# Optimization experiments

Measured on AMD Instinct MI355X. Metric: run time of the kernel, lower is better.

The kernel has to match this reference:

```python
import jax, jax.numpy as jnp
import numpy as np

N = 100000     # nodes
E = 1600000    # directed edges
IN, HID, OUT = 128, 64, 64


def setup_inputs() -> dict:
    key = jax.random.key(0)
    k = jax.random.split(key, 6)
    features = jax.random.normal(k[0], (N, IN), dtype=jnp.float32)
    edge_index = jax.random.randint(k[1], (2, E), 0, N, dtype=jnp.int64)
    # Glorot-ish init for linear weights, zeros for bias (PyG GCNConv default)
    W1 = jax.random.normal(k[2], (IN, HID), dtype=jnp.float32) / np.sqrt(IN)
    b1 = jnp.zeros((HID,), dtype=jnp.float32)
    W2 = jax.random.normal(k[3], (HID, OUT), dtype=jnp.float32) / np.sqrt(HID)
    b2 = jnp.zeros((OUT,), dtype=jnp.float32)
    return {"features": features, "edge_index": edge_index, "batch_size": N,
            "W1": W1, "b1": b1, "W2": W2, "b2": b2}


def _gcn_conv(x, W, b, src, dst, n):
    """PyG GCNConv: add self-loops, symmetric deg^-1/2 normalization,
    linear transform then scatter-add aggregation, plus bias."""
    loops = jnp.arange(n, dtype=src.dtype)
    s = jnp.concatenate([src, loops])   # [E+N]
    d = jnp.concatenate([dst, loops])   # [E+N]
    deg = jax.ops.segment_sum(jnp.ones(s.shape, dtype=x.dtype), d, num_segments=n)
    dinv = jnp.where(deg > 0, jax.lax.rsqrt(deg), jnp.zeros_like(deg))
    norm = dinv[s] * dinv[d]            # [E+N]
    h = x @ W                           # [n, out] transform before aggregation
    msg = h[s] * norm[:, None]          # gather + scale  [E+N, out]
    out = jax.ops.segment_sum(msg, d, num_segments=n)  # scatter-add
    return out + b


def reference(features, edge_index, batch_size, W1, b1, W2, b2):
    src, dst = edge_index[0], edge_index[1]
    n = features.shape[0]
    x = _gcn_conv(features, W1, b1, src, dst, n)
    x = jax.nn.relu(x)
    # F.dropout(training=self.training): module is in eval mode -> identity
    x = _gcn_conv(x, W2, b2, src, dst, n)
    return jax.nn.log_softmax(x, axis=1)
```

## Files before the change

kernel.cpp:

```cpp
#include <hip/hip_runtime.h>
#include <hip/hip_fp16.h>
#include <math.h>

#define K1 128
#define C  64
#define SCAN_B 1024

__global__ void detect_kernel(const int* __restrict__ e, int twoE, int* __restrict__ flag) {
    __shared__ int nz;
    if (threadIdx.x == 0) nz = 0;
    __syncthreads();
    int nchk = twoE / 2; if (nchk > 4096) nchk = 4096;
    int bad = 0;
    for (int i = threadIdx.x; i < nchk; i += blockDim.x)
        if (e[2 * i + 1] != 0) bad = 1;
    if (bad) atomicOr(&nz, 1);
    __syncthreads();
    if (threadIdx.x == 0) *flag = nz ? 0 : 1;
}

__device__ __forceinline__ int load_dst(const void* EI, int E, int e, int is64) {
    return is64 ? (int)((const long long*)EI)[(size_t)E + e] : ((const int*)EI)[(size_t)E + e];
}
__device__ __forceinline__ int load_src(const void* EI, int E, int e, int is64) {
    return is64 ? (int)((const long long*)EI)[e] : ((const int*)EI)[e];
}

__global__ __launch_bounds__(256) void hist_kernel(const void* __restrict__ EI, int E,
        const int* __restrict__ flag, int* __restrict__ cnt) {
    const int is64 = *flag;
    for (int e = blockIdx.x * 256 + threadIdx.x; e < E; e += gridDim.x * 256)
        atomicAdd(&cnt[load_dst(EI, E, e, is64)], 1);
}

__global__ __launch_bounds__(SCAN_B) void scan1_kernel(const int* __restrict__ cnt, int n,
        int* __restrict__ ex, int* __restrict__ bsum, float* __restrict__ dinv) {
    __shared__ int s[SCAN_B];
    int i = blockIdx.x * SCAN_B + threadIdx.x;
    int v = (i < n) ? cnt[i] : 0;
    s[threadIdx.x] = v;
    __syncthreads();
    for (int off = 1; off < SCAN_B; off <<= 1) {
        int t = (threadIdx.x >= off) ? s[threadIdx.x - off] : 0;
        __syncthreads();
        s[threadIdx.x] += t;
        __syncthreads();
    }
    if (i < n) {
        ex[i] = s[threadIdx.x] - v;
        dinv[i] = rsqrtf((float)(v + 1));
    }
    if (threadIdx.x == SCAN_B - 1) bsum[blockIdx.x] = s[SCAN_B - 1];
}

__global__ void scan2_kernel(int* __restrict__ bsum, int nb) {
    const int lane = threadIdx.x & 63;
    int acc = 0;
    for (int base = 0; base < nb; base += 64) {
        int v = (base + lane < nb) ? bsum[base + lane] : 0;
        int sc = v;
        #pragma unroll
        for (int off = 1; off < 64; off <<= 1) {
            int t = __shfl_up(sc, off, 64);
            if (lane >= off) sc += t;
        }
        if (base + lane < nb) bsum[base + lane] = acc + sc - v;
        acc += __shfl(sc, 63, 64);
    }
}

__global__ void scan3_kernel(int* __restrict__ ex, const int* __restrict__ bsum,
                             int* __restrict__ fill, int n, int Etot) {
    for (int i = blockIdx.x * blockDim.x + threadIdx.x; i < n; i += gridDim.x * blockDim.x) {
        int v = ex[i] + bsum[i / SCAN_B];
        ex[i] = v;
        fill[i] = v;
    }
    if (blockIdx.x == 0 && threadIdx.x == 0) ex[n] = Etot;
}

__global__ __launch_bounds__(256) void scatter_kernel(const void* __restrict__ EI, int E,
        const int* __restrict__ flag, int* __restrict__ fill, int* __restrict__ csr) {
    const int is64 = *flag;
    for (int e = blockIdx.x * 256 + threadIdx.x; e < E; e += gridDim.x * 256) {
        int d = load_dst(EI, E, e, is64);
        int s = load_src(EI, E, e, is64);
        int pos = atomicAdd(&fill[d], 1);
        csr[pos] = s;
    }
}

template<int K, int R>
__global__ __launch_bounds__(256) void gemm_kernel(const float* __restrict__ X,
        const float* __restrict__ W, const float* __restrict__ dinv,
        __half* __restrict__ G, int n)
{
    __shared__ float Ws[K * C];
    for (int i = threadIdx.x; i < K * C; i += 256) Ws[i] = W[i];
    __syncthreads();
    const int lane = threadIdx.x & 63;
    const int wave = __builtin_amdgcn_readfirstlane((int)(threadIdx.x >> 6));
    const int waves = gridDim.x * 4;
    for (int base = (blockIdx.x * 4 + wave) * R; base < n; base += waves * R) {
        float acc[R];
        #pragma unroll
        for (int r = 0; r < R; ++r) acc[r] = 0.0f;
        if (base + R <= n) {
            for (int k = 0; k < K; ++k) {
                float w = Ws[k * C + lane];
                #pragma unroll
                for (int r = 0; r < R; ++r)
                    acc[r] = fmaf(X[(size_t)(base + r) * K + k], w, acc[r]);
            }
            #pragma unroll
            for (int r = 0; r < R; ++r)
                G[(size_t)(base + r) * C + lane] = __float2half_rn(acc[r] * dinv[base + r]);
        } else {
            for (int r = 0; r < R; ++r) {
                if (base + r >= n) break;
                float a = 0.0f;
                for (int k = 0; k < K; ++k)
                    a = fmaf(X[(size_t)(base + r) * K + k], Ws[k * C + lane], a);
                G[(size_t)(base + r) * C + lane] = __float2half_rn(a * dinv[base + r]);
            }
        }
    }
}

__global__ __launch_bounds__(256) void gather_fused_kernel(const int* __restrict__ rowptr,
        const int* __restrict__ csr, const __half* __restrict__ G,
        const float* __restrict__ dinv, const float* __restrict__ b1,
        const float* __restrict__ W2, __half* __restrict__ G2, int n)
{
    __shared__ __align__(16) float Hrow[4][C];
    const int lane = threadIdx.x & 63;
    const int wv = __builtin_amdgcn_readfirstlane((int)(threadIdx.x >> 6));
    float w[C];
    #pragma unroll
    for (int k = 0; k < C; ++k) w[k] = W2[k * C + lane];
    const float bias = b1[lane];
    const int nwaves = gridDim.x * 4;
    for (int v = __builtin_amdgcn_readfirstlane(blockIdx.x * 4 + wv); v < n; v += nwaves) {
        const int start = __builtin_amdgcn_readfirstlane(rowptr[v]);
        const int end   = __builtin_amdgcn_readfirstlane(rowptr[v + 1]);
        float a0 = __half2float(G[(size_t)v * C + lane]);
        float a1 = 0.f, a2 = 0.f, a3 = 0.f;
        for (int base = start; base < end; base += 64) {
            int m = end - base; if (m > 64) m = 64;
            int idx = (lane < m) ? csr[base + lane] : 0;
            int j = 0;
            for (; j + 4 <= m; j += 4) {
                int s0 = __shfl(idx, j,     64);
                int s1 = __shfl(idx, j + 1, 64);
                int s2 = __shfl(idx, j + 2, 64);
                int s3 = __shfl(idx, j + 3, 64);
                a0 += __half2float(G[(size_t)s0 * C + lane]);
                a1 += __half2float(G[(size_t)s1 * C + lane]);
                a2 += __half2float(G[(size_t)s2 * C + lane]);
                a3 += __half2float(G[(size_t)s3 * C + lane]);
            }
            for (; j < m; ++j) {
                int s = __shfl(idx, j, 64);
                a0 += __half2float(G[(size_t)s * C + lane]);
            }
        }
        float y = fmaf((a0 + a1) + (a2 + a3), dinv[v], bias);
        y = y > 0.f ? y : 0.f;
        Hrow[wv][lane] = y;
        float o = 0.f;
        #pragma unroll
        for (int k0 = 0; k0 < C / 4; ++k0) {
            float4 h4 = *(const float4*)&Hrow[wv][k0 * 4];
            o = fmaf(h4.x, w[4 * k0 + 0], o);
            o = fmaf(h4.y, w[4 * k0 + 1], o);
            o = fmaf(h4.z, w[4 * k0 + 2], o);
            o = fmaf(h4.w, w[4 * k0 + 3], o);
        }
        G2[(size_t)v * C + lane] = __float2half_rn(o * dinv[v]);
    }
}

__global__ __launch_bounds__(256) void gather_ls_kernel(const int* __restrict__ rowptr,
        const int* __restrict__ csr, const __half* __restrict__ G,
        const float* __restrict__ dinv, const float* __restrict__ bias,
        float* __restrict__ Out, int n)
{
    const int lane = threadIdx.x & 63;
    const int v = __builtin_amdgcn_readfirstlane((int)(blockIdx.x * 4 + (threadIdx.x >> 6)));
    if (v >= n) return;
    const int start = __builtin_amdgcn_readfirstlane(rowptr[v]);
    const int end   = __builtin_amdgcn_readfirstlane(rowptr[v + 1]);
    float a0 = __half2float(G[(size_t)v * C + lane]);
    float a1 = 0.f, a2 = 0.f, a3 = 0.f;
    for (int base = start; base < end; base += 64) {
        int m = end - base; if (m > 64) m = 64;
        int idx = (lane < m) ? csr[base + lane] : 0;
        int j = 0;
        for (; j + 4 <= m; j += 4) {
            int s0 = __shfl(idx, j,     64);
            int s1 = __shfl(idx, j + 1, 64);
            int s2 = __shfl(idx, j + 2, 64);
            int s3 = __shfl(idx, j + 3, 64);
            a0 += __half2float(G[(size_t)s0 * C + lane]);
            a1 += __half2float(G[(size_t)s1 * C + lane]);
            a2 += __half2float(G[(size_t)s2 * C + lane]);
            a3 += __half2float(G[(size_t)s3 * C + lane]);
        }
        for (; j < m; ++j) {
            int s = __shfl(idx, j, 64);
            a0 += __half2float(G[(size_t)s * C + lane]);
        }
    }
    float y = fmaf((a0 + a1) + (a2 + a3), dinv[v], bias[lane]);
    float mx = y;
    #pragma unroll
    for (int off = 32; off > 0; off >>= 1) mx = fmaxf(mx, __shfl_xor(mx, off, 64));
    float ex = expf(y - mx);
    float l = ex;
    #pragma unroll
    for (int off = 32; off > 0; off >>= 1) l += __shfl_xor(l, off, 64);
    Out[(size_t)v * C + lane] = y - mx - logf(l);
}

static inline size_t align16(size_t x) { return (x + 15) & ~(size_t)15; }

extern "C" void kernel_launch(void* const* d_in, const int* in_sizes, int n_in,
                              void* d_out, int out_size, void* d_ws, size_t ws_size,
                              hipStream_t stream)
{
    const float* X  = (const float*)d_in[0];
    const void*  EI = d_in[1];
    const float* W1 = (const float*)d_in[3];
    const float* b1 = (const float*)d_in[4];
    const float* W2 = (const float*)d_in[5];
    const float* b2 = (const float*)d_in[6];
    float* Out = (float*)d_out;

    const int n    = in_sizes[0] / K1;
    const int E    = in_sizes[1] / 2;
    const int twoE = 2 * E;
    const int nb   = (n + SCAN_B - 1) / SCAN_B;

    char* ws = (char*)d_ws;
    size_t off = 0;
    int*    csr    = (int*)(ws + off);    off = align16(off + (size_t)E * 4);
    int*    rowptr = (int*)(ws + off);    off = align16(off + (size_t)(n + 1) * 4);
    int*    cnt    = (int*)(ws + off);    off = align16(off + (size_t)n * 4);
    int*    bsum   = (int*)(ws + off);    off = align16(off + (size_t)(nb + 1) * 4);
    int*    flag   = (int*)(ws + off);    off = align16(off + 16);
    float*  dinv   = (float*)(ws + off);  off = align16(off + (size_t)n * 4);
    __half* G      = (__half*)(ws + off); off = align16(off + (size_t)n * C * 2);
    __half* G2     = (__half*)(ws + off); off = align16(off + (size_t)n * C * 2);
    int*    fill   = cnt;

    hipLaunchKernelGGL(detect_kernel, dim3(1), dim3(256), 0, stream, (const int*)EI, twoE, flag);
    hipMemsetAsync(cnt, 0, (size_t)n * 4, stream);

    hipLaunchKernelGGL(hist_kernel,  dim3(1024), dim3(256), 0, stream, EI, E, flag, cnt);
    hipLaunchKernelGGL(scan1_kernel, dim3(nb), dim3(SCAN_B), 0, stream, cnt, n, rowptr, bsum, dinv);
    hipLaunchKernelGGL(scan2_kernel, dim3(1), dim3(64), 0, stream, bsum, nb);
    hipLaunchKernelGGL(scan3_kernel, dim3(1024), dim3(256), 0, stream, rowptr, bsum, fill, n, E);
    hipLaunchKernelGGL(scatter_kernel, dim3(2048), dim3(256), 0, stream, EI, E, flag, fill, csr);

    hipLaunchKernelGGL((gemm_kernel<K1, 8>), dim3(2048), dim3(256), 0, stream, X, W1, dinv, G, n);
    hipLaunchKernelGGL(gather_fused_kernel, dim3(2048), dim3(256), 0, stream,
                       rowptr, csr, G, dinv, b1, W2, G2, n);
    const int ngb = (n + 3) / 4;
    hipLaunchKernelGGL(gather_ls_kernel, dim3(ngb), dim3(256), 0, stream,
                       rowptr, csr, G2, dinv, b2, Out, n);
}
```

Before: 524.7 us.

## Partition histogram and CSR scatter by destination range; unroll gathers by eight

The histogram and scatter kernels now split blocks into eight groups. Each group scans every edge but only performs atomics for destinations in its own node range, which is meant to keep the atomic targets cache-local and reduce contention, at the cost of reading the edge list eight times. The gather loops in both aggregation kernels are shared through a macro and unrolled to eight independent loads and accumulators, to raise memory-level parallelism.

New measurement: 484.2 us. 1.08x faster.

```diff
diff --git a/kernel.cpp b/kernel.cpp
--- a/kernel.cpp
+++ b/kernel.cpp
@@ -5,6 +5,7 @@
 #define K1 128
 #define C  64
 #define SCAN_B 1024
+#define NPART 8
 
 __global__ void detect_kernel(const int* __restrict__ e, int twoE, int* __restrict__ flag) {
     __shared__ int nz;
@@ -27,10 +28,17 @@
 }
 
 __global__ __launch_bounds__(256) void hist_kernel(const void* __restrict__ EI, int E,
-        const int* __restrict__ flag, int* __restrict__ cnt) {
+        const int* __restrict__ flag, int* __restrict__ cnt, int n) {
     const int is64 = *flag;
-    for (int e = blockIdx.x * 256 + threadIdx.x; e < E; e += gridDim.x * 256)
-        atomicAdd(&cnt[load_dst(EI, E, e, is64)], 1);
+    const int part = blockIdx.x & (NPART - 1);
+    const int span = (n + NPART - 1) / NPART;
+    const int lo = part * span;
+    const int hi = (lo + span < n) ? lo + span : n;
+    const int blk = blockIdx.x >> 3, nblk = gridDim.x >> 3;
+    for (int e = blk * 256 + threadIdx.x; e < E; e += nblk * 256) {
+        int d = load_dst(EI, E, e, is64);
+        if (d >= lo && d < hi) atomicAdd(&cnt[d], 1);
+    }
 }
 
 __global__ __launch_bounds__(SCAN_B) void scan1_kernel(const int* __restrict__ cnt, int n,
@@ -80,13 +88,21 @@
 }
 
 __global__ __launch_bounds__(256) void scatter_kernel(const void* __restrict__ EI, int E,
-        const int* __restrict__ flag, int* __restrict__ fill, int* __restrict__ csr) {
+        const int* __restrict__ flag, int* __restrict__ fill, int* __restrict__ csr,
+        int n) {
     const int is64 = *flag;
-    for (int e = blockIdx.x * 256 + threadIdx.x; e < E; e += gridDim.x * 256) {
+    const int part = blockIdx.x & (NPART - 1);
+    const int span = (n + NPART - 1) / NPART;
+    const int lo = part * span;
+    const int hi = (lo + span < n) ? lo + span : n;
+    const int blk = blockIdx.x >> 3, nblk = gridDim.x >> 3;
+    for (int e = blk * 256 + threadIdx.x; e < E; e += nblk * 256) {
         int d = load_dst(EI, E, e, is64);
-        int s = load_src(EI, E, e, is64);
-        int pos = atomicAdd(&fill[d], 1);
-        csr[pos] = s;
+        if (d >= lo && d < hi) {
+            int s = load_src(EI, E, e, is64);
+            int pos = atomicAdd(&fill[d], 1);
+            csr[pos] = s;
+        }
     }
 }
 
@@ -127,6 +143,38 @@
     }
 }
 
+#define GATHER_ROW(G_, start_, end_)                                          \
+    float a0 = __half2float(G_[(size_t)v * C + lane]);                        \
+    float a1 = 0.f, a2 = 0.f, a3 = 0.f, a4 = 0.f, a5 = 0.f, a6 = 0.f, a7 = 0.f; \
+    for (int base = start_; base < end_; base += 64) {                        \
+        int m = end_ - base; if (m > 64) m = 64;                              \
+        int idx = (lane < m) ? csr[base + lane] : 0;                          \
+        int j = 0;                                                            \
+        for (; j + 8 <= m; j += 8) {                                          \
+            int s0 = __shfl(idx, j,     64);                                  \
+            int s1 = __shfl(idx, j + 1, 64);                                  \
+            int s2 = __shfl(idx, j + 2, 64);                                  \
+            int s3 = __shfl(idx, j + 3, 64);                                  \
+            int s4 = __shfl(idx, j + 4, 64);                                  \
+            int s5 = __shfl(idx, j + 5, 64);                                  \
+            int s6 = __shfl(idx, j + 6, 64);                                  \
+            int s7 = __shfl(idx, j + 7, 64);                                  \
+            a0 += __half2float(G_[(size_t)s0 * C + lane]);                    \
+            a1 += __half2float(G_[(size_t)s1 * C + lane]);                    \
+            a2 += __half2float(G_[(size_t)s2 * C + lane]);                    \
+            a3 += __half2float(G_[(size_t)s3 * C + lane]);                    \
+            a4 += __half2float(G_[(size_t)s4 * C + lane]);                    \
+            a5 += __half2float(G_[(size_t)s5 * C + lane]);                    \
+            a6 += __half2float(G_[(size_t)s6 * C + lane]);                    \
+            a7 += __half2float(G_[(size_t)s7 * C + lane]);                    \
+        }                                                                     \
+        for (; j < m; ++j) {                                                  \
+            int s = __shfl(idx, j, 64);                                       \
+            a0 += __half2float(G_[(size_t)s * C + lane]);                     \
+        }                                                                     \
+    }                                                                         \
+    float acc = ((a0 + a1) + (a2 + a3)) + ((a4 + a5) + (a6 + a7));
+
 __global__ __launch_bounds__(256) void gather_fused_kernel(const int* __restrict__ rowptr,
         const int* __restrict__ csr, const __half* __restrict__ G,
         const float* __restrict__ dinv, const float* __restrict__ b1,
@@ -143,28 +191,8 @@
     for (int v = __builtin_amdgcn_readfirstlane(blockIdx.x * 4 + wv); v < n; v += nwaves) {
         const int start = __builtin_amdgcn_readfirstlane(rowptr[v]);
         const int end   = __builtin_amdgcn_readfirstlane(rowptr[v + 1]);
-        float a0 = __half2float(G[(size_t)v * C + lane]);
-        float a1 = 0.f, a2 = 0.f, a3 = 0.f;
-        for (int base = start; base < end; base += 64) {
-            int m = end - base; if (m > 64) m = 64;
-            int idx = (lane < m) ? csr[base + lane] : 0;
-            int j = 0;
-            for (; j + 4 <= m; j += 4) {
-                int s0 = __shfl(idx, j,     64);
-                int s1 = __shfl(idx, j + 1, 64);
-                int s2 = __shfl(idx, j + 2, 64);
-                int s3 = __shfl(idx, j + 3, 64);
-                a0 += __half2float(G[(size_t)s0 * C + lane]);
-                a1 += __half2float(G[(size_t)s1 * C + lane]);
-                a2 += __half2float(G[(size_t)s2 * C + lane]);
-                a3 += __half2float(G[(size_t)s3 * C + lane]);
-            }
-            for (; j < m; ++j) {
-                int s = __shfl(idx, j, 64);
-                a0 += __half2float(G[(size_t)s * C + lane]);
-            }
-        }
-        float y = fmaf((a0 + a1) + (a2 + a3), dinv[v], bias);
+        GATHER_ROW(G, start, end)
+        float y = fmaf(acc, dinv[v], bias);
         y = y > 0.f ? y : 0.f;
         Hrow[wv][lane] = y;
         float o = 0.f;
@@ -181,7 +209,7 @@
 }
 
 __global__ __launch_bounds__(256) void gather_ls_kernel(const int* __restrict__ rowptr,
-        const int* __restrict__ csr, const __half* __restrict__ G,
+        const int* __restrict__ csr, const __half* __restrict__ G2,
         const float* __restrict__ dinv, const float* __restrict__ bias,
         float* __restrict__ Out, int n)
 {
@@ -190,28 +218,8 @@
     if (v >= n) return;
     const int start = __builtin_amdgcn_readfirstlane(rowptr[v]);
     const int end   = __builtin_amdgcn_readfirstlane(rowptr[v + 1]);
-    float a0 = __half2float(G[(size_t)v * C + lane]);
-    float a1 = 0.f, a2 = 0.f, a3 = 0.f;
-    for (int base = start; base < end; base += 64) {
-        int m = end - base; if (m > 64) m = 64;
-        int idx = (lane < m) ? csr[base + lane] : 0;
-        int j = 0;
-        for (; j + 4 <= m; j += 4) {
-            int s0 = __shfl(idx, j,     64);
-            int s1 = __shfl(idx, j + 1, 64);
-            int s2 = __shfl(idx, j + 2, 64);
-            int s3 = __shfl(idx, j + 3, 64);
-            a0 += __half2float(G[(size_t)s0 * C + lane]);
-            a1 += __half2float(G[(size_t)s1 * C + lane]);
-            a2 += __half2float(G[(size_t)s2 * C + lane]);
-            a3 += __half2float(G[(size_t)s3 * C + lane]);
-        }
-        for (; j < m; ++j) {
-            int s = __shfl(idx, j, 64);
-            a0 += __half2float(G[(size_t)s * C + lane]);
-        }
-    }
-    float y = fmaf((a0 + a1) + (a2 + a3), dinv[v], bias[lane]);
+    GATHER_ROW(G2, start, end)
+    float y = fmaf(acc, dinv[v], bias[lane]);
     float mx = y;
     #pragma unroll
     for (int off = 32; off > 0; off >>= 1) mx = fmaxf(mx, __shfl_xor(mx, off, 64));
@@ -256,11 +264,11 @@
     hipLaunchKernelGGL(detect_kernel, dim3(1), dim3(256), 0, stream, (const int*)EI, twoE, flag);
     hipMemsetAsync(cnt, 0, (size_t)n * 4, stream);
 
-    hipLaunchKernelGGL(hist_kernel,  dim3(1024), dim3(256), 0, stream, EI, E, flag, cnt);
+    hipLaunchKernelGGL(hist_kernel,  dim3(2048), dim3(256), 0, stream, EI, E, flag, cnt, n);
     hipLaunchKernelGGL(scan1_kernel, dim3(nb), dim3(SCAN_B), 0, stream, cnt, n, rowptr, bsum, dinv);
     hipLaunchKernelGGL(scan2_kernel, dim3(1), dim3(64), 0, stream, bsum, nb);
     hipLaunchKernelGGL(scan3_kernel, dim3(1024), dim3(256), 0, stream, rowptr, bsum, fill, n, E);
-    hipLaunchKernelGGL(scatter_kernel, dim3(2048), dim3(256), 0, stream, EI, E, flag, fill, csr);
+    hipLaunchKernelGGL(scatter_kernel, dim3(2048), dim3(256), 0, stream, EI, E, flag, fill, csr, n);
 
     hipLaunchKernelGGL((gemm_kernel<K1, 8>), dim3(2048), dim3(256), 0, stream, X, W1, dinv, G, n);
     hipLaunchKernelGGL(gather_fused_kernel, dim3(2048), dim3(256), 0, stream,
```
